# Kernel tuning notes

Hardware: AMD Instinct MI355X
Metric: run time of the kernel (lower is better)

Reference implementation:

```python
import jax, jax.numpy as jnp
import numpy as np

NUM_ENVS = 16384
N = 12          # decision vars (4 legs x 3D force)
M_CON = 24      # 4 SOC cones (3 each) + 12-dim hardtanh box
A_MIN, A_MAX = -10.0, 10.0
ALPHA, BETA = 1.0, 1.0


def setup_inputs() -> dict:
    key = jax.random.key(0)
    k1, k2, k3, k4 = jax.random.split(key, 4)
    Mw = jax.random.normal(k1, (NUM_ENVS, N, N), dtype=jnp.float32) / np.sqrt(N)
    # P must be SPD for inv/solve as in the original QP setup
    P = Mw @ jnp.swapaxes(Mw, -1, -2) + jnp.eye(N, dtype=jnp.float32)
    q = jax.random.normal(k2, (NUM_ENVS, N), dtype=jnp.float32)
    H = jax.random.normal(k3, (NUM_ENVS, M_CON, N), dtype=jnp.float32) * 0.5
    b = jax.random.normal(k4, (NUM_ENVS, M_CON), dtype=jnp.float32)
    contact_filter = jnp.ones((NUM_ENVS, M_CON), dtype=jnp.float32)
    return {"P": P, "q": q, "H": H, "b": b, "contact_filter": contact_filter, "iters": 100}


def _project(z, cf):
    # z: [B, m, 1]. Faithful to torch: project_onto_soc's only in-place effect on z
    # is z_part *= (z_part[:, 2:3] > 0); the full cone projection result is
    # discarded (returned but never written back). Then hardtanh box, then contact filter.
    Bsz = z.shape[0]
    soc = z[:, :12].reshape(Bsz, 4, 3)               # 4 cones of dim 3
    soc = soc * (soc[:, :, 2:3] > 0)                 # zero cone block if z-component <= 0
    box = jnp.clip(z[:, 12:24], A_MIN, A_MAX)        # hardtanh
    z = jnp.concatenate([soc.reshape(Bsz, 12, 1), box], axis=1)
    return z * cf


def reference(P, q, H, b, contact_filter, iters):
    m = H.shape[1]
    q_ = q[..., None]                                # [B, n, 1]
    b_ = b[..., None]                                # [B, m, 1]
    cf = contact_filter[..., None]                   # [B, m, 1]
    Ht = jnp.swapaxes(H, -1, -2)
    I = jnp.eye(m, dtype=P.dtype)
    Fm = I - H @ jnp.linalg.inv(P + Ht @ H) @ Ht     # [B, m, m]
    mu = Fm @ (H @ jnp.linalg.solve(P, q_) - b_)     # [B, m, 1]
    A = jnp.concatenate([
        jnp.concatenate([Fm, BETA * Fm], axis=2),
        jnp.concatenate([ALPHA * (I - 2.0 * Fm), I - 2.0 * ALPHA * BETA * Fm], axis=2),
    ], axis=1)                                       # [B, 2m, 2m]
    Bv = jnp.concatenate([BETA * mu, -2.0 * ALPHA * BETA * mu], axis=1)  # [B, 2m, 1]

    def step(lz, _):
        lz = A @ lz + Bv
        lz = jnp.concatenate([lz[:, :m], _project(lz[:, m:], cf)], axis=1)
        return lz, None

    lz0 = jnp.zeros((P.shape[0], 2 * m, 1), dtype=P.dtype)
    lz, _ = jax.lax.scan(step, lz0, None, length=iters)
    x = jnp.linalg.pinv(H) @ (lz[:, m:] - b_)        # [B, n, 1]
    return x, lz
```

## Files before the change

### kernel.cpp

```cpp
#include <hip/hip_runtime.h>

#define EPB 32
#define BLOCK 256
#define HS 292
#define GS 148
#define SS 28

#define WFENCE() __builtin_amdgcn_wave_barrier()

#define DPP_XOR1 0xB1
#define DPP_XOR2 0x4E
#define DPP_HMIR 0x141

constexpr int GMAP[8] = {0, 1, 2, 3, 7, 6, 5, 4};

typedef float f2 __attribute__((ext_vector_type(2)));

__device__ __forceinline__ f2 pkfma(f2 a, f2 b, f2 c) {
  return __builtin_elementwise_fma(a, b, c);
}

#define FMA4(acc, f, s)                                         \
  acc = fmaf((f).x, (s).x,                                      \
        fmaf((f).y, (s).y,                                      \
        fmaf((f).z, (s).z,                                      \
        fmaf((f).w, (s).w, (acc)))))

#define VFMA(acc, s, v)                                         \
  { (acc).x = fmaf((s), (v).x, (acc).x);                        \
    (acc).y = fmaf((s), (v).y, (acc).y);                        \
    (acc).z = fmaf((s), (v).z, (acc).z);                        \
    (acc).w = fmaf((s), (v).w, (acc).w); }

#define ADD4(A, B) { (A).x += (B).x; (A).y += (B).y; (A).z += (B).z; (A).w += (B).w; }

template<int CTRL>
__device__ __forceinline__ float dppv(float v) {
  return __int_as_float(__builtin_amdgcn_update_dpp(
      0, __float_as_int(v), CTRL, 0xF, 0xF, true));
}

template<int K>
__device__ __forceinline__ float getel(const float4& a, const float4& b, const float4& c) {
  if constexpr (K == 0) return a.x; else if constexpr (K == 1) return a.y;
  else if constexpr (K == 2) return a.z; else if constexpr (K == 3) return a.w;
  else if constexpr (K == 4) return b.x; else if constexpr (K == 5) return b.y;
  else if constexpr (K == 6) return b.z; else if constexpr (K == 7) return b.w;
  else if constexpr (K == 8) return c.x; else if constexpr (K == 9) return c.y;
  else if constexpr (K == 10) return c.z; else return c.w;
}
template<int K>
__device__ __forceinline__ void setel(float4& a, float4& b, float4& c, float v) {
  if constexpr (K == 0) a.x = v; else if constexpr (K == 1) a.y = v;
  else if constexpr (K == 2) a.z = v; else if constexpr (K == 3) a.w = v;
  else if constexpr (K == 4) b.x = v; else if constexpr (K == 5) b.y = v;
  else if constexpr (K == 6) b.z = v; else if constexpr (K == 7) b.w = v;
  else if constexpr (K == 8) c.x = v; else if constexpr (K == 9) c.y = v;
  else if constexpr (K == 10) c.z = v; else c.w = v;
}

template<int S>
__device__ __forceinline__ void putS2(f2* m, float v) {
  if constexpr ((S & 1) == 0) m[S / 2].x = v; else m[S / 2].y = v;
}

#define PMQ(pm, Q) make_float4(pm[2*(Q)].x, pm[2*(Q)].y, pm[2*(Q)+1].x, pm[2*(Q)+1].y)

__device__ __forceinline__ float dot12(float4 a0, float4 a1, float4 a2,
                                       const float* p) {
  const float4* p4 = (const float4*)p;
  float4 b0 = p4[0], b1 = p4[1], b2 = p4[2];
  float acc = 0.f;
  FMA4(acc, a0, b0); FMA4(acc, a1, b1); FMA4(acc, a2, b2);
  return acc;
}

template<int K>
__device__ __forceinline__ void pivot_pub(float4& a, float4& b, float4& c, float* piv) {
  float ip = 1.0f / getel<K>(a, b, c);
  setel<K>(a, b, c, 1.0f);
  a.x *= ip; a.y *= ip; a.z *= ip; a.w *= ip;
  b.x *= ip; b.y *= ip; b.z *= ip; b.w *= ip;
  c.x *= ip; c.y *= ip; c.z *= ip; c.w *= ip;
  float4* pv = (float4*)piv;
  pv[0] = a; pv[1] = b; pv[2] = c;
}

#define ELIM(f, A, B, C)                                              \
  { (A).x = fmaf(-(f), p0.x, (A).x); (A).y = fmaf(-(f), p0.y, (A).y); \
    (A).z = fmaf(-(f), p0.z, (A).z); (A).w = fmaf(-(f), p0.w, (A).w); \
    (B).x = fmaf(-(f), p1.x, (B).x); (B).y = fmaf(-(f), p1.y, (B).y); \
    (B).z = fmaf(-(f), p1.z, (B).z); (B).w = fmaf(-(f), p1.w, (B).w); \
    (C).x = fmaf(-(f), p2.x, (C).x); (C).y = fmaf(-(f), p2.y, (C).y); \
    (C).z = fmaf(-(f), p2.z, (C).z); (C).w = fmaf(-(f), p2.w, (C).w); }

template<int K>
__device__ __forceinline__ void rgj_step(float4& a0, float4& b0, float4& c0,
                                         float4& a1, float4& b1, float4& c1,
                                         float* piv, int t) {
  if constexpr (K < 8) {
    if (t == K) pivot_pub<K>(a0, b0, c0, piv);
  } else {
    if (t == K - 8) pivot_pub<K>(a1, b1, c1, piv);
  }
  WFENCE();
  const float4* pv = (const float4*)piv;
  float4 p0 = pv[0], p1 = pv[1], p2 = pv[2];
  {
    const bool own = (K < 8) && (t == K);
    float cur = getel<K>(a0, b0, c0);
    float f = own ? 0.0f : cur;
    setel<K>(a0, b0, c0, own ? cur : 0.0f);
    ELIM(f, a0, b0, c0);
  }
  {
    const bool own = (K >= 8) && (t == K - 8);
    float cur = getel<K>(a1, b1, c1);
    float f = own ? 0.0f : cur;
    setel<K>(a1, b1, c1, own ? cur : 0.0f);
    ELIM(f, a1, b1, c1);
  }
  WFENCE();
}

template<int K>
__device__ __forceinline__ void rgj_all(float4& a0, float4& b0, float4& c0,
                                        float4& a1, float4& b1, float4& c1,
                                        float* piv, int t) {
  rgj_step<K>(a0, b0, c0, a1, b1, c1, piv, t);
  if constexpr (K < 11) rgj_all<K + 1>(a0, b0, c0, a1, b1, c1, piv, t);
}

__device__ __forceinline__ void gram_rows(const float* myH, int t, int i1,
    float4& a0, float4& b0, float4& c0, float4& a1, float4& b1, float4& c1) {
  a0 = make_float4(0.f, 0.f, 0.f, 0.f);
  b0 = a0; c0 = a0; a1 = a0; b1 = a0; c1 = a0;
#pragma unroll
  for (int k = 0; k < 24; ++k) {
    const float4* hk = (const float4*)(myH + k * 12);
    float4 h0 = hk[0], h1 = hk[1], h2 = hk[2];
    float f0 = myH[k * 12 + t];
    float f1 = myH[k * 12 + i1];
    VFMA(a0, f0, h0); VFMA(b0, f0, h1); VFMA(c0, f0, h2);
    VFMA(a1, f1, h0); VFMA(b1, f1, h1); VFMA(c1, f1, h2);
  }
}

template<int g, int k>
__device__ __forceinline__ void slot3(const float* myH, int t,
    const float4* W0, const float4* W1, const float4* W2,
    f2* P0, f2* P1, f2* P2) {
  const int c = 3 * (t ^ GMAP[g]) + k;
  const float4* hc = (const float4*)(myH + c * 12);
  float4 h0 = hc[0], h1 = hc[1], h2 = hc[2];
  float d0 = 0.f, d1 = 0.f, d2 = 0.f;
  FMA4(d0, h0, W0[0]); FMA4(d0, h1, W0[1]); FMA4(d0, h2, W0[2]);
  FMA4(d1, h0, W1[0]); FMA4(d1, h1, W1[1]); FMA4(d1, h2, W1[2]);
  FMA4(d2, h0, W2[0]); FMA4(d2, h1, W2[1]); FMA4(d2, h2, W2[2]);
  constexpr int S = 3 * g + k;
  putS2<S>(P0, ((g == 0 && k == 0) ? 1.0f : 0.0f) - d0);
  putS2<S>(P1, ((g == 0 && k == 1) ? 1.0f : 0.0f) - d1);
  putS2<S>(P2, ((g == 0 && k == 2) ? 1.0f : 0.0f) - d2);
}

template<int S>
__device__ __forceinline__ float bgat(const float* bB, int t) {
  constexpr int g = S / 3, k = S % 3;
  return bB[3 * (t ^ GMAP[g]) + k];
}

__global__ __attribute__((amdgpu_flat_work_group_size(BLOCK, BLOCK),
                          amdgpu_waves_per_eu(1, 4)))
void pdhg_kernel(const float* __restrict__ P, const float* __restrict__ q,
                 const float* __restrict__ H, const float* __restrict__ b,
                 const float* __restrict__ cf, const int* __restrict__ itp,
                 float* __restrict__ out, int Btot) {
  __shared__ __align__(16) float sH[EPB * HS];
  __shared__ __align__(16) float sGi[EPB * GS];
  __shared__ __align__(16) float sB[EPB * SS];
  __shared__ __align__(16) float sAux[EPB * SS];

  const int tid  = threadIdx.x;
  const int wq   = tid >> 6;
  const int lane = tid & 63;
  const int e    = wq * 8 + (lane >> 3);
  const int t    = lane & 7;
  const int env  = blockIdx.x * EPB + e;
  const int envW0 = blockIdx.x * EPB + wq * 8;
  const int niter = itp[0];
  const int r0w = 3 * t;
  const int i1 = (t < 4) ? t + 8 : t;

  {
    const float4* gH = (const float4*)(H + (size_t)envW0 * 288);
#pragma unroll
    for (int rep = 0; rep < 9; ++rep) {
      int i = lane + rep * 64;
      int ee = i / 72, off = i - ee * 72;
      *(float4*)&sH[(wq * 8 + ee) * HS + off * 4] = gH[i];
    }
    const float4* gP = (const float4*)(P + (size_t)envW0 * 144);
#pragma unroll
    for (int rep = 0; rep < 4; ++rep) {
      int i = lane + rep * 64;
      int ee = i / 36, off = i - ee * 36;
      *(float4*)&sGi[(wq * 8 + ee) * GS + off * 4] = gP[i];
    }
    { int i = lane + 256; if (lane < 32) {
        int ee = i / 36, off = i - ee * 36;
        *(float4*)&sGi[(wq * 8 + ee) * GS + off * 4] = gP[i]; } }
    const float4* gq = (const float4*)(q + (size_t)envW0 * 12);
    if (lane < 24) {
      int ee = lane / 3, off = lane - ee * 3;
      *(float4*)&sAux[(wq * 8 + ee) * SS + off * 4] = gq[lane];
    }
    const float4* gb = (const float4*)(b + (size_t)envW0 * 24);
    if (lane < 48) {
      int ee = lane / 6, off = lane - ee * 6;
      *(float4*)&sB[(wq * 8 + ee) * SS + off * 4] = gb[lane];
    }
  }
  WFENCE();

  const float* myH = &sH[e * HS];
  float* giB  = &sGi[e * GS];
  float* auxB = &sAux[e * SS];
  float* bBm  = &sB[e * SS];
  const float* bB = bBm;

  float4 g0a, g0b, g0c, g1a, g1b, g1c;
  gram_rows(myH, t, i1, g0a, g0b, g0c, g1a, g1b, g1c);
  {
    const float4* p0 = (const float4*)(giB + t * 12);
    const float4* p1 = (const float4*)(giB + i1 * 12);
    float4 q0 = p0[0], q1 = p0[1], q2 = p0[2];
    float4 r0 = p1[0], r1 = p1[1], r2 = p1[2];
    ADD4(g0a, q0); ADD4(g0b, q1); ADD4(g0c, q2);
    ADD4(g1a, r0); ADD4(g1b, r1); ADD4(g1c, r2);
  }
  rgj_all<0>(g0a, g0b, g0c, g1a, g1b, g1c, auxB + 12, t);

  {
    float4* w0 = (float4*)(giB + t * 12);
    w0[0] = g0a; w0[1] = g0b; w0[2] = g0c;
    if (t < 4) {
      float4* w1 = (float4*)(giB + (t + 8) * 12);
      w1[0] = g1a; w1[1] = g1b; w1[2] = g1c;
    }
  }
  float y0 = dot12(g0a, g0b, g0c, auxB);
  float y1 = dot12(g1a, g1b, g1c, auxB);
  WFENCE();
  auxB[12 + t] = y0;
  if (t < 4) auxB[20 + t] = y1;
  WFENCE();

  float4 hr0[3], hr1[3], hr2[3];
  { const float4* p = (const float4*)(myH + (r0w + 0) * 12); hr0[0]=p[0]; hr0[1]=p[1]; hr0[2]=p[2]; }
  { const float4* p = (const float4*)(myH + (r0w + 1) * 12); hr1[0]=p[0]; hr1[1]=p[1]; hr1[2]=p[2]; }
  { const float4* p = (const float4*)(myH + (r0w + 2) * 12); hr2[0]=p[0]; hr2[1]=p[1]; hr2[2]=p[2]; }
  float u0, u1, u2;
  {
    const float4* y4 = (const float4*)(auxB + 12);
    float4 ya = y4[0], yb = y4[1], yc = y4[2];
    u0 = 0.f; FMA4(u0, hr0[0], ya); FMA4(u0, hr0[1], yb); FMA4(u0, hr0[2], yc);
    u1 = 0.f; FMA4(u1, hr1[0], ya); FMA4(u1, hr1[1], yb); FMA4(u1, hr1[2], yc);
    u2 = 0.f; FMA4(u2, hr2[0], ya); FMA4(u2, hr2[1], yb); FMA4(u2, hr2[2], yc);
  }

  float4 W0[3], W1[3], W2[3];
  W0[0] = make_float4(0.f,0.f,0.f,0.f); W0[1] = W0[0]; W0[2] = W0[0];
  W1[0] = W0[0]; W1[1] = W0[0]; W1[2] = W0[0];
  W2[0] = W0[0]; W2[1] = W0[0]; W2[2] = W0[0];
#define ACC_W(c, EX)                                                   \
  { const float4* g4 = (const float4*)(giB + (c) * 12);                \
    float4 r0 = g4[0], r1 = g4[1], r2 = g4[2];                         \
    float k0 = hr0[(c) >> 2].EX, k1 = hr1[(c) >> 2].EX, k2 = hr2[(c) >> 2].EX; \
    VFMA(W0[0], k0, r0); VFMA(W0[1], k0, r1); VFMA(W0[2], k0, r2);     \
    VFMA(W1[0], k1, r0); VFMA(W1[1], k1, r1); VFMA(W1[2], k1, r2);     \
    VFMA(W2[0], k2, r0); VFMA(W2[1], k2, r1); VFMA(W2[2], k2, r2); }
  ACC_W(0, x) ACC_W(1, y) ACC_W(2,  z) ACC_W(3,  w)
  ACC_W(4, x) ACC_W(5, y) ACC_W(6,  z) ACC_W(7,  w)
  ACC_W(8, x) ACC_W(9, y) ACC_W(10, z) ACC_W(11, w)
#undef ACC_W

  f2 pm0[12], pm1[12], pm2[12];
#define SL(g, k) slot3<g, k>(myH, t, W0, W1, W2, pm0, pm1, pm2);
  SL(0,0) SL(0,1) SL(0,2)  SL(1,0) SL(1,1) SL(1,2)
  SL(2,0) SL(2,1) SL(2,2)  SL(3,0) SL(3,1) SL(3,2)
  SL(4,0) SL(4,1) SL(4,2)  SL(5,0) SL(5,1) SL(5,2)
  SL(6,0) SL(6,1) SL(6,2)  SL(7,0) SL(7,1) SL(7,2)
#undef SL

  float mu0, mu1, mu2;
  {
    float4 bg0 = make_float4(bgat<0>(bB,t),  bgat<1>(bB,t),  bgat<2>(bB,t),  bgat<3>(bB,t));
    float4 bg1 = make_float4(bgat<4>(bB,t),  bgat<5>(bB,t),  bgat<6>(bB,t),  bgat<7>(bB,t));
    float4 bg2 = make_float4(bgat<8>(bB,t),  bgat<9>(bB,t),  bgat<10>(bB,t), bgat<11>(bB,t));
    float4 bg3 = make_float4(bgat<12>(bB,t), bgat<13>(bB,t), bgat<14>(bB,t), bgat<15>(bB,t));
    float4 bg4 = make_float4(bgat<16>(bB,t), bgat<17>(bB,t), bgat<18>(bB,t), bgat<19>(bB,t));
    float4 bg5 = make_float4(bgat<20>(bB,t), bgat<21>(bB,t), bgat<22>(bB,t), bgat<23>(bB,t));
    float d0 = 0.f, d1 = 0.f, d2 = 0.f;
    FMA4(d0, PMQ(pm0,0), bg0); FMA4(d1, PMQ(pm1,0), bg0); FMA4(d2, PMQ(pm2,0), bg0);
    FMA4(d0, PMQ(pm0,1), bg1); FMA4(d1, PMQ(pm1,1), bg1); FMA4(d2, PMQ(pm2,1), bg1);
    FMA4(d0, PMQ(pm0,2), bg2); FMA4(d1, PMQ(pm1,2), bg2); FMA4(d2, PMQ(pm2,2), bg2);
    FMA4(d0, PMQ(pm0,3), bg3); FMA4(d1, PMQ(pm1,3), bg3); FMA4(d2, PMQ(pm2,3), bg3);
    FMA4(d0, PMQ(pm0,4), bg4); FMA4(d1, PMQ(pm1,4), bg4); FMA4(d2, PMQ(pm2,4), bg4);
    FMA4(d0, PMQ(pm0,5), bg5); FMA4(d1, PMQ(pm1,5), bg5); FMA4(d2, PMQ(pm2,5), bg5);
    mu0 = u0 - d0;
    mu1 = u1 - d1;
    mu2 = u2 - d2;
  }
  float cfr0 = cf[(size_t)env * 24 + r0w];
  float cfr1 = cf[(size_t)env * 24 + r0w + 1];
  float cfr2 = cf[(size_t)env * 24 + r0w + 2];

  const float plo  = (t < 4) ? -3.0e38f : -10.0f;
  const float phi  = (t < 4) ?  3.0e38f :  10.0f;
  const float pthr = (t < 4) ? 0.0f     : -3.0e38f;
  float l0 = 0.f, l1 = 0.f, l2 = 0.f, z0 = 0.f, z1 = 0.f, z2 = 0.f;
#pragma unroll 2
  for (int it = 0; it < niter; ++it) {
    float s0 = l0 + z0, s1 = l1 + z1, s2 = l2 + z2;
    float g3  = dppv<DPP_XOR1>(s0), g4  = dppv<DPP_XOR1>(s1), g5  = dppv<DPP_XOR1>(s2);
    float g6  = dppv<DPP_XOR2>(s0), g7  = dppv<DPP_XOR2>(s1), g8  = dppv<DPP_XOR2>(s2);
    float g12 = dppv<DPP_HMIR>(s0), g13 = dppv<DPP_HMIR>(s1), g14 = dppv<DPP_HMIR>(s2);
    f2 vp0 = {s0, s1};
    f2 A0 = {mu0, 0.f}, A1 = {mu1, 0.f}, A2 = {mu2, 0.f};
    A0 = pkfma(pm0[0], vp0, A0); A1 = pkfma(pm1[0], vp0, A1); A2 = pkfma(pm2[0], vp0, A2);
    float g9  = dppv<DPP_XOR2>(g3),  g10 = dppv<DPP_XOR2>(g4),  g11 = dppv<DPP_XOR2>(g5);
    float g15 = dppv<DPP_HMIR>(g3),  g16 = dppv<DPP_HMIR>(g4),  g17 = dppv<DPP_HMIR>(g5);
    float g18 = dppv<DPP_HMIR>(g6),  g19 = dppv<DPP_HMIR>(g7),  g20 = dppv<DPP_HMIR>(g8);
    f2 vp1 = {s2, g3}, vp2 = {g4, g5}, vp3 = {g6, g7};
    A0 = pkfma(pm0[1], vp1, A0); A1 = pkfma(pm1[1], vp1, A1); A2 = pkfma(pm2[1], vp1, A2);
    A0 = pkfma(pm0[2], vp2, A0); A1 = pkfma(pm1[2], vp2, A1); A2 = pkfma(pm2[2], vp2, A2);
    A0 = pkfma(pm0[3], vp3, A0); A1 = pkfma(pm1[3], vp3, A1); A2 = pkfma(pm2[3], vp3, A2);
    float g21 = dppv<DPP_HMIR>(g9), g22 = dppv<DPP_HMIR>(g10), g23 = dppv<DPP_HMIR>(g11);
    f2 vp4 = {g8, g9}, vp5 = {g10, g11};
    A0 = pkfma(pm0[4], vp4, A0); A1 = pkfma(pm1[4], vp4, A1); A2 = pkfma(pm2[4], vp4, A2);
    A0 = pkfma(pm0[5], vp5, A0); A1 = pkfma(pm1[5], vp5, A1); A2 = pkfma(pm2[5], vp5, A2);
    f2 vp6 = {g12, g13}, vp7 = {g14, g15}, vp8 = {g16, g17}, vp9 = {g18, g19};
    f2 B0 = {0.f, 0.f}, B1 = {0.f, 0.f}, B2 = {0.f, 0.f};
    B0 = pkfma(pm0[6], vp6, B0); B1 = pkfma(pm1[6], vp6, B1); B2 = pkfma(pm2[6], vp6, B2);
    B0 = pkfma(pm0[7], vp7, B0); B1 = pkfma(pm1[7], vp7, B1); B2 = pkfma(pm2[7], vp7, B2);
    B0 = pkfma(pm0[8], vp8, B0); B1 = pkfma(pm1[8], vp8, B1); B2 = pkfma(pm2[8], vp8, B2);
    B0 = pkfma(pm0[9], vp9, B0); B1 = pkfma(pm1[9], vp9, B1); B2 = pkfma(pm2[9], vp9, B2);
    f2 vp10 = {g20, g21}, vp11 = {g22, g23};
    B0 = pkfma(pm0[10], vp10, B0); B1 = pkfma(pm1[10], vp10, B1); B2 = pkfma(pm2[10], vp10, B2);
    B0 = pkfma(pm0[11], vp11, B0); B1 = pkfma(pm1[11], vp11, B1); B2 = pkfma(pm2[11], vp11, B2);
    f2 C0 = A0 + B0, C1 = A1 + B1, C2 = A2 + B2;
    float w0 = C0.x + C0.y, w1 = C1.x + C1.y, w2 = C2.x + C2.y;
    float zp0 = fmaf(-2.0f, w0, s0);
    float zp1 = fmaf(-2.0f, w1, s1);
    float zp2 = fmaf(-2.0f, w2, s2);
    l0 = w0; l1 = w1; l2 = w2;
    bool gt = zp2 > pthr;
    float e0 = gt ? cfr0 : 0.0f;
    float e1 = gt ? cfr1 : 0.0f;
    float e2 = gt ? cfr2 : 0.0f;
    z0 = __builtin_amdgcn_fmed3f(zp0, plo, phi) * e0;
    z1 = __builtin_amdgcn_fmed3f(zp1, plo, phi) * e1;
    z2 = __builtin_amdgcn_fmed3f(zp2, plo, phi) * e2;
  }

  float* xout  = out;
  float* lzout = out + (size_t)Btot * 12;
  lzout[(size_t)env * 48 + r0w]          = l0;
  lzout[(size_t)env * 48 + r0w + 1]      = l1;
  lzout[(size_t)env * 48 + r0w + 2]      = l2;
  lzout[(size_t)env * 48 + 24 + r0w]     = z0;
  lzout[(size_t)env * 48 + 24 + r0w + 1] = z1;
  lzout[(size_t)env * 48 + 24 + r0w + 2] = z2;

  float bo0 = bB[r0w];
  float bo1 = bB[r0w + 1];
  float bo2 = bB[r0w + 2];
  WFENCE();
  auxB[r0w]     = z0 - bo0;
  auxB[r0w + 1] = z1 - bo1;
  auxB[r0w + 2] = z2 - bo2;
  WFENCE();

  float rv0 = 0.f, rv8 = 0.f;
  {
    const float4* a4 = (const float4*)auxB;
    float4 au0 = a4[0], au1 = a4[1], au2 = a4[2], au3 = a4[3], au4 = a4[4], au5 = a4[5];
#define RVS(k, AV) { rv0 = fmaf(myH[(k) * 12 + t],  (AV), rv0);   \
                     rv8 = fmaf(myH[(k) * 12 + i1], (AV), rv8); }
    RVS(0,  au0.x) RVS(1,  au0.y) RVS(2,  au0.z) RVS(3,  au0.w)
    RVS(4,  au1.x) RVS(5,  au1.y) RVS(6,  au1.z) RVS(7,  au1.w)
    RVS(8,  au2.x) RVS(9,  au2.y) RVS(10, au2.z) RVS(11, au2.w)
    RVS(12, au3.x) RVS(13, au3.y) RVS(14, au3.z) RVS(15, au3.w)
    RVS(16, au4.x) RVS(17, au4.y) RVS(18, au4.z) RVS(19, au4.w)
    RVS(20, au5.x) RVS(21, au5.y) RVS(22, au5.z) RVS(23, au5.w)
#undef RVS
  }

  gram_rows(myH, t, i1, g0a, g0b, g0c, g1a, g1b, g1c);
  WFENCE();
  auxB[t] = rv0;
  if (t < 4) auxB[t + 8] = rv8;
  WFENCE();
  rgj_all<0>(g0a, g0b, g0c, g1a, g1b, g1c, bBm, t);

  xout[(size_t)env * 12 + t] = dot12(g0a, g0b, g0c, auxB);
  if (t < 4)
    xout[(size_t)env * 12 + t + 8] = dot12(g1a, g1b, g1c, auxB);
}

extern "C" void kernel_launch(void* const* d_in, const int* in_sizes, int n_in,
                              void* d_out, int out_size, void* d_ws, size_t ws_size,
                              hipStream_t stream) {
  const float* P  = (const float*)d_in[0];
  const float* q  = (const float*)d_in[1];
  const float* H  = (const float*)d_in[2];
  const float* b  = (const float*)d_in[3];
  const float* cf = (const float*)d_in[4];
  const int*   it = (const int*)d_in[5];
  float* out = (float*)d_out;
  const int B = in_sizes[1] / 12;
  const int grid = B / EPB;
  pdhg_kernel<<<grid, BLOCK, 0, stream>>>(P, q, H, b, cf, it, out, B);
}
```

Measured before the change: 139.6 us.

## Process two environments per lane group to interleave independent iteration chains

Each 8-lane group now handles two environments (A and B) instead of one, with the block shrunk to 128 threads so EPB stays 32. The 100-step iteration interleaves the two environments' DPP shuffles and packed FMAs to hide latency through instruction-level parallelism. The DPP gather also changes: g9..g11 come from a single quad-permute DPP on s instead of a chained XOR2 of g3, which shortens the dependency chain. In exchange, per-thread register pressure roughly doubles (two sets of 36 packed coefficients), which may lower occupancy or cause spills, and there are half as many threads per block.

Result: slower. 182.2 us (+30.6%).

```diff
diff --git a/kernel.cpp b/kernel.cpp
--- a/kernel.cpp
+++ b/kernel.cpp
@@ -1,7 +1,7 @@
 #include <hip/hip_runtime.h>
 
 #define EPB 32
-#define BLOCK 256
+#define BLOCK 128
 #define HS 292
 #define GS 148
 #define SS 28
@@ -10,6 +10,7 @@
 
 #define DPP_XOR1 0xB1
 #define DPP_XOR2 0x4E
+#define DPP_QP3  0x1B
 #define DPP_HMIR 0x141
 
 constexpr int GMAP[8] = {0, 1, 2, 3, 7, 6, 5, 4};
@@ -169,6 +170,197 @@
   return bB[3 * (t ^ GMAP[g]) + k];
 }
 
+struct ES {
+  f2 pm0[12], pm1[12], pm2[12];
+  float mu0, mu1, mu2;
+  float cf0, cf1, cf2;
+  float l0, l1, l2, z0, z1, z2;
+};
+
+__device__ __forceinline__ void build_env(ES& S, const float* myH, float* gi,
+                                          float* aux, const float* bB,
+                                          const float* cfp, int t, int i1, int r0w) {
+  float4 g0a, g0b, g0c, g1a, g1b, g1c;
+  gram_rows(myH, t, i1, g0a, g0b, g0c, g1a, g1b, g1c);
+  {
+    const float4* p0 = (const float4*)(gi + t * 12);
+    const float4* p1 = (const float4*)(gi + i1 * 12);
+    float4 q0 = p0[0], q1 = p0[1], q2 = p0[2];
+    float4 r0 = p1[0], r1 = p1[1], r2 = p1[2];
+    ADD4(g0a, q0); ADD4(g0b, q1); ADD4(g0c, q2);
+    ADD4(g1a, r0); ADD4(g1b, r1); ADD4(g1c, r2);
+  }
+  rgj_all<0>(g0a, g0b, g0c, g1a, g1b, g1c, aux + 12, t);
+  {
+    float4* w0 = (float4*)(gi + t * 12);
+    w0[0] = g0a; w0[1] = g0b; w0[2] = g0c;
+    if (t < 4) {
+      float4* w1 = (float4*)(gi + (t + 8) * 12);
+      w1[0] = g1a; w1[1] = g1b; w1[2] = g1c;
+    }
+  }
+  float y0 = dot12(g0a, g0b, g0c, aux);
+  float y1 = dot12(g1a, g1b, g1c, aux);
+  WFENCE();
+  aux[12 + t] = y0;
+  if (t < 4) aux[20 + t] = y1;
+  WFENCE();
+
+  float4 hr0[3], hr1[3], hr2[3];
+  { const float4* p = (const float4*)(myH + (r0w + 0) * 12); hr0[0]=p[0]; hr0[1]=p[1]; hr0[2]=p[2]; }
+  { const float4* p = (const float4*)(myH + (r0w + 1) * 12); hr1[0]=p[0]; hr1[1]=p[1]; hr1[2]=p[2]; }
+  { const float4* p = (const float4*)(myH + (r0w + 2) * 12); hr2[0]=p[0]; hr2[1]=p[1]; hr2[2]=p[2]; }
+  float u0, u1, u2;
+  {
+    const float4* y4 = (const float4*)(aux + 12);
+    float4 ya = y4[0], yb = y4[1], yc = y4[2];
+    u0 = 0.f; FMA4(u0, hr0[0], ya); FMA4(u0, hr0[1], yb); FMA4(u0, hr0[2], yc);
+    u1 = 0.f; FMA4(u1, hr1[0], ya); FMA4(u1, hr1[1], yb); FMA4(u1, hr1[2], yc);
+    u2 = 0.f; FMA4(u2, hr2[0], ya); FMA4(u2, hr2[1], yb); FMA4(u2, hr2[2], yc);
+  }
+
+  float4 W0[3], W1[3], W2[3];
+  W0[0] = make_float4(0.f,0.f,0.f,0.f); W0[1] = W0[0]; W0[2] = W0[0];
+  W1[0] = W0[0]; W1[1] = W0[0]; W1[2] = W0[0];
+  W2[0] = W0[0]; W2[1] = W0[0]; W2[2] = W0[0];
+#define ACC_W(c, EX)                                                   \
+  { const float4* g4 = (const float4*)(gi + (c) * 12);                 \
+    float4 r0 = g4[0], r1 = g4[1], r2 = g4[2];                         \
+    float k0 = hr0[(c) >> 2].EX, k1 = hr1[(c) >> 2].EX, k2 = hr2[(c) >> 2].EX; \
+    VFMA(W0[0], k0, r0); VFMA(W0[1], k0, r1); VFMA(W0[2], k0, r2);     \
+    VFMA(W1[0], k1, r0); VFMA(W1[1], k1, r1); VFMA(W1[2], k1, r2);     \
+    VFMA(W2[0], k2, r0); VFMA(W2[1], k2, r1); VFMA(W2[2], k2, r2); }
+  ACC_W(0, x) ACC_W(1, y) ACC_W(2,  z) ACC_W(3,  w)
+  ACC_W(4, x) ACC_W(5, y) ACC_W(6,  z) ACC_W(7,  w)
+  ACC_W(8, x) ACC_W(9, y) ACC_W(10, z) ACC_W(11, w)
+#undef ACC_W
+
+#define SL(g, k) slot3<g, k>(myH, t, W0, W1, W2, S.pm0, S.pm1, S.pm2);
+  SL(0,0) SL(0,1) SL(0,2)  SL(1,0) SL(1,1) SL(1,2)
+  SL(2,0) SL(2,1) SL(2,2)  SL(3,0) SL(3,1) SL(3,2)
+  SL(4,0) SL(4,1) SL(4,2)  SL(5,0) SL(5,1) SL(5,2)
+  SL(6,0) SL(6,1) SL(6,2)  SL(7,0) SL(7,1) SL(7,2)
+#undef SL
+
+  {
+    float4 bg0 = make_float4(bgat<0>(bB,t),  bgat<1>(bB,t),  bgat<2>(bB,t),  bgat<3>(bB,t));
+    float4 bg1 = make_float4(bgat<4>(bB,t),  bgat<5>(bB,t),  bgat<6>(bB,t),  bgat<7>(bB,t));
+    float4 bg2 = make_float4(bgat<8>(bB,t),  bgat<9>(bB,t),  bgat<10>(bB,t), bgat<11>(bB,t));
+    float4 bg3 = make_float4(bgat<12>(bB,t), bgat<13>(bB,t), bgat<14>(bB,t), bgat<15>(bB,t));
+    float4 bg4 = make_float4(bgat<16>(bB,t), bgat<17>(bB,t), bgat<18>(bB,t), bgat<19>(bB,t));
+    float4 bg5 = make_float4(bgat<20>(bB,t), bgat<21>(bB,t), bgat<22>(bB,t), bgat<23>(bB,t));
+    float d0 = 0.f, d1 = 0.f, d2 = 0.f;
+    FMA4(d0, PMQ(S.pm0,0), bg0); FMA4(d1, PMQ(S.pm1,0), bg0); FMA4(d2, PMQ(S.pm2,0), bg0);
+    FMA4(d0, PMQ(S.pm0,1), bg1); FMA4(d1, PMQ(S.pm1,1), bg1); FMA4(d2, PMQ(S.pm2,1), bg1);
+    FMA4(d0, PMQ(S.pm0,2), bg2); FMA4(d1, PMQ(S.pm1,2), bg2); FMA4(d2, PMQ(S.pm2,2), bg2);
+    FMA4(d0, PMQ(S.pm0,3), bg3); FMA4(d1, PMQ(S.pm1,3), bg3); FMA4(d2, PMQ(S.pm2,3), bg3);
+    FMA4(d0, PMQ(S.pm0,4), bg4); FMA4(d1, PMQ(S.pm1,4), bg4); FMA4(d2, PMQ(S.pm2,4), bg4);
+    FMA4(d0, PMQ(S.pm0,5), bg5); FMA4(d1, PMQ(S.pm1,5), bg5); FMA4(d2, PMQ(S.pm2,5), bg5);
+    S.mu0 = u0 - d0;
+    S.mu1 = u1 - d1;
+    S.mu2 = u2 - d2;
+  }
+  S.cf0 = cfp[0]; S.cf1 = cfp[1]; S.cf2 = cfp[2];
+  S.l0 = S.l1 = S.l2 = S.z0 = S.z1 = S.z2 = 0.f;
+}
+
+__device__ __forceinline__ void epi_env(ES& S, const float* myH, float* gi,
+                                        float* aux, float* bBm,
+                                        float* xout, float* lzout,
+                                        int env_, int t, int i1, int r0w) {
+  lzout[(size_t)env_ * 48 + r0w]          = S.l0;
+  lzout[(size_t)env_ * 48 + r0w + 1]      = S.l1;
+  lzout[(size_t)env_ * 48 + r0w + 2]      = S.l2;
+  lzout[(size_t)env_ * 48 + 24 + r0w]     = S.z0;
+  lzout[(size_t)env_ * 48 + 24 + r0w + 1] = S.z1;
+  lzout[(size_t)env_ * 48 + 24 + r0w + 2] = S.z2;
+
+  float bo0 = bBm[r0w];
+  float bo1 = bBm[r0w + 1];
+  float bo2 = bBm[r0w + 2];
+  WFENCE();
+  aux[r0w]     = S.z0 - bo0;
+  aux[r0w + 1] = S.z1 - bo1;
+  aux[r0w + 2] = S.z2 - bo2;
+  WFENCE();
+
+  float rv0 = 0.f, rv8 = 0.f;
+  {
+    const float4* a4 = (const float4*)aux;
+    float4 au0 = a4[0], au1 = a4[1], au2 = a4[2], au3 = a4[3], au4 = a4[4], au5 = a4[5];
+#define RVS(k, AV) { rv0 = fmaf(myH[(k) * 12 + t],  (AV), rv0);   \
+                     rv8 = fmaf(myH[(k) * 12 + i1], (AV), rv8); }
+    RVS(0,  au0.x) RVS(1,  au0.y) RVS(2,  au0.z) RVS(3,  au0.w)
+    RVS(4,  au1.x) RVS(5,  au1.y) RVS(6,  au1.z) RVS(7,  au1.w)
+    RVS(8,  au2.x) RVS(9,  au2.y) RVS(10, au2.z) RVS(11, au2.w)
+    RVS(12, au3.x) RVS(13, au3.y) RVS(14, au3.z) RVS(15, au3.w)
+    RVS(16, au4.x) RVS(17, au4.y) RVS(18, au4.z) RVS(19, au4.w)
+    RVS(20, au5.x) RVS(21, au5.y) RVS(22, au5.z) RVS(23, au5.w)
+#undef RVS
+  }
+
+  float4 g0a, g0b, g0c, g1a, g1b, g1c;
+  gram_rows(myH, t, i1, g0a, g0b, g0c, g1a, g1b, g1c);
+  WFENCE();
+  aux[t] = rv0;
+  if (t < 4) aux[t + 8] = rv8;
+  WFENCE();
+  rgj_all<0>(g0a, g0b, g0c, g1a, g1b, g1c, bBm, t);
+
+  xout[(size_t)env_ * 12 + t] = dot12(g0a, g0b, g0c, aux);
+  if (t < 4)
+    xout[(size_t)env_ * 12 + t + 8] = dot12(g1a, g1b, g1c, aux);
+}
+
+#define IT_S(E) \
+  float E##s0 = E.l0 + E.z0, E##s1 = E.l1 + E.z1, E##s2 = E.l2 + E.z2;
+
+#define IT_L1(E) \
+  float E##g3  = dppv<DPP_XOR1>(E##s0), E##g4  = dppv<DPP_XOR1>(E##s1), E##g5  = dppv<DPP_XOR1>(E##s2); \
+  float E##g6  = dppv<DPP_XOR2>(E##s0), E##g7  = dppv<DPP_XOR2>(E##s1), E##g8  = dppv<DPP_XOR2>(E##s2); \
+  float E##g9  = dppv<DPP_QP3>(E##s0),  E##g10 = dppv<DPP_QP3>(E##s1),  E##g11 = dppv<DPP_QP3>(E##s2);  \
+  float E##g12 = dppv<DPP_HMIR>(E##s0), E##g13 = dppv<DPP_HMIR>(E##s1), E##g14 = dppv<DPP_HMIR>(E##s2);
+
+#define IT_L2(E) \
+  float E##g15 = dppv<DPP_HMIR>(E##g3), E##g16 = dppv<DPP_HMIR>(E##g4), E##g17 = dppv<DPP_HMIR>(E##g5); \
+  float E##g18 = dppv<DPP_HMIR>(E##g6), E##g19 = dppv<DPP_HMIR>(E##g7), E##g20 = dppv<DPP_HMIR>(E##g8); \
+  float E##g21 = dppv<DPP_HMIR>(E##g9), E##g22 = dppv<DPP_HMIR>(E##g10), E##g23 = dppv<DPP_HMIR>(E##g11);
+
+#define IT_FMA(E) \
+  f2 E##vp0 = {E##s0, E##s1},   E##vp1 = {E##s2, E##g3},   E##vp2 = {E##g4, E##g5};   \
+  f2 E##vp3 = {E##g6, E##g7},   E##vp4 = {E##g8, E##g9},   E##vp5 = {E##g10, E##g11}; \
+  f2 E##vp6 = {E##g12, E##g13}, E##vp7 = {E##g14, E##g15}, E##vp8 = {E##g16, E##g17}; \
+  f2 E##vp9 = {E##g18, E##g19}, E##vp10 = {E##g20, E##g21}, E##vp11 = {E##g22, E##g23}; \
+  f2 E##A0 = {E.mu0, 0.f}, E##A1 = {E.mu1, 0.f}, E##A2 = {E.mu2, 0.f}; \
+  f2 E##B0 = {0.f, 0.f}, E##B1 = {0.f, 0.f}, E##B2 = {0.f, 0.f}; \
+  E##A0 = pkfma(E.pm0[0], E##vp0, E##A0); E##A1 = pkfma(E.pm1[0], E##vp0, E##A1); E##A2 = pkfma(E.pm2[0], E##vp0, E##A2); \
+  E##A0 = pkfma(E.pm0[1], E##vp1, E##A0); E##A1 = pkfma(E.pm1[1], E##vp1, E##A1); E##A2 = pkfma(E.pm2[1], E##vp1, E##A2); \
+  E##A0 = pkfma(E.pm0[2], E##vp2, E##A0); E##A1 = pkfma(E.pm1[2], E##vp2, E##A1); E##A2 = pkfma(E.pm2[2], E##vp2, E##A2); \
+  E##A0 = pkfma(E.pm0[3], E##vp3, E##A0); E##A1 = pkfma(E.pm1[3], E##vp3, E##A1); E##A2 = pkfma(E.pm2[3], E##vp3, E##A2); \
+  E##A0 = pkfma(E.pm0[4], E##vp4, E##A0); E##A1 = pkfma(E.pm1[4], E##vp4, E##A1); E##A2 = pkfma(E.pm2[4], E##vp4, E##A2); \
+  E##A0 = pkfma(E.pm0[5], E##vp5, E##A0); E##A1 = pkfma(E.pm1[5], E##vp5, E##A1); E##A2 = pkfma(E.pm2[5], E##vp5, E##A2); \
+  E##B0 = pkfma(E.pm0[6], E##vp6, E##B0); E##B1 = pkfma(E.pm1[6], E##vp6, E##B1); E##B2 = pkfma(E.pm2[6], E##vp6, E##B2); \
+  E##B0 = pkfma(E.pm0[7], E##vp7, E##B0); E##B1 = pkfma(E.pm1[7], E##vp7, E##B1); E##B2 = pkfma(E.pm2[7], E##vp7, E##B2); \
+  E##B0 = pkfma(E.pm0[8], E##vp8, E##B0); E##B1 = pkfma(E.pm1[8], E##vp8, E##B1); E##B2 = pkfma(E.pm2[8], E##vp8, E##B2); \
+  E##B0 = pkfma(E.pm0[9], E##vp9, E##B0); E##B1 = pkfma(E.pm1[9], E##vp9, E##B1); E##B2 = pkfma(E.pm2[9], E##vp9, E##B2); \
+  E##B0 = pkfma(E.pm0[10], E##vp10, E##B0); E##B1 = pkfma(E.pm1[10], E##vp10, E##B1); E##B2 = pkfma(E.pm2[10], E##vp10, E##B2); \
+  E##B0 = pkfma(E.pm0[11], E##vp11, E##B0); E##B1 = pkfma(E.pm1[11], E##vp11, E##B1); E##B2 = pkfma(E.pm2[11], E##vp11, E##B2);
+
+#define IT_TAIL(E) \
+  f2 E##C0 = E##A0 + E##B0, E##C1 = E##A1 + E##B1, E##C2 = E##A2 + E##B2; \
+  float E##w0 = E##C0.x + E##C0.y, E##w1 = E##C1.x + E##C1.y, E##w2 = E##C2.x + E##C2.y; \
+  float E##zp0 = fmaf(-2.0f, E##w0, E##s0); \
+  float E##zp1 = fmaf(-2.0f, E##w1, E##s1); \
+  float E##zp2 = fmaf(-2.0f, E##w2, E##s2); \
+  E.l0 = E##w0; E.l1 = E##w1; E.l2 = E##w2; \
+  bool E##gt = E##zp2 > pthr; \
+  float E##e0 = E##gt ? E.cf0 : 0.0f; \
+  float E##e1 = E##gt ? E.cf1 : 0.0f; \
+  float E##e2 = E##gt ? E.cf2 : 0.0f; \
+  E.z0 = __builtin_amdgcn_fmed3f(E##zp0, plo, phi) * E##e0; \
+  E.z1 = __builtin_amdgcn_fmed3f(E##zp1, plo, phi) * E##e1; \
+  E.z2 = __builtin_amdgcn_fmed3f(E##zp2, plo, phi) * E##e2;
+
 __global__ __attribute__((amdgpu_flat_work_group_size(BLOCK, BLOCK),
                           amdgpu_waves_per_eu(1, 4)))
 void pdhg_kernel(const float* __restrict__ P, const float* __restrict__ q,
@@ -183,10 +375,13 @@
   const int tid  = threadIdx.x;
   const int wq   = tid >> 6;
   const int lane = tid & 63;
-  const int e    = wq * 8 + (lane >> 3);
+  const int g8   = lane >> 3;
   const int t    = lane & 7;
-  const int env  = blockIdx.x * EPB + e;
-  const int envW0 = blockIdx.x * EPB + wq * 8;
+  const int eA   = wq * 16 + g8;
+  const int eB   = eA + 8;
+  const int envA = blockIdx.x * EPB + eA;
+  const int envB = envA + 8;
+  const int envW0 = blockIdx.x * EPB + wq * 16;
   const int niter = itp[0];
   const int r0w = 3 * t;
   const int i1 = (t < 4) ? t + 8 : t;
@@ -194,218 +389,66 @@
   {
     const float4* gH = (const float4*)(H + (size_t)envW0 * 288);
 #pragma unroll
-    for (int rep = 0; rep < 9; ++rep) {
+    for (int rep = 0; rep < 18; ++rep) {
       int i = lane + rep * 64;
       int ee = i / 72, off = i - ee * 72;
-      *(float4*)&sH[(wq * 8 + ee) * HS + off * 4] = gH[i];
+      *(float4*)&sH[(wq * 16 + ee) * HS + off * 4] = gH[i];
     }
     const float4* gP = (const float4*)(P + (size_t)envW0 * 144);
 #pragma unroll
-    for (int rep = 0; rep < 4; ++rep) {
+    for (int rep = 0; rep < 9; ++rep) {
       int i = lane + rep * 64;
       int ee = i / 36, off = i - ee * 36;
-      *(float4*)&sGi[(wq * 8 + ee) * GS + off * 4] = gP[i];
+      *(float4*)&sGi[(wq * 16 + ee) * GS + off * 4] = gP[i];
     }
-    { int i = lane + 256; if (lane < 32) {
-        int ee = i / 36, off = i - ee * 36;
-        *(float4*)&sGi[(wq * 8 + ee) * GS + off * 4] = gP[i]; } }
     const float4* gq = (const float4*)(q + (size_t)envW0 * 12);
-    if (lane < 24) {
+    if (lane < 48) {
       int ee = lane / 3, off = lane - ee * 3;
-      *(float4*)&sAux[(wq * 8 + ee) * SS + off * 4] = gq[lane];
+      *(float4*)&sAux[(wq * 16 + ee) * SS + off * 4] = gq[lane];
     }
     const float4* gb = (const float4*)(b + (size_t)envW0 * 24);
-    if (lane < 48) {
-      int ee = lane / 6, off = lane - ee * 6;
-      *(float4*)&sB[(wq * 8 + ee) * SS + off * 4] = gb[lane];
+    {
+      int i = lane;
+      int ee = i / 6, off = i - ee * 6;
+      *(float4*)&sB[(wq * 16 + ee) * SS + off * 4] = gb[i];
+      if (lane < 32) {
+        i = lane + 64;
+        ee = i / 6; off = i - ee * 6;
+        *(float4*)&sB[(wq * 16 + ee) * SS + off * 4] = gb[i];
+      }
     }
   }
   WFENCE();
 
-  const float* myH = &sH[e * HS];
-  float* giB  = &sGi[e * GS];
-  float* auxB = &sAux[e * SS];
-  float* bBm  = &sB[e * SS];
-  const float* bB = bBm;
-
-  float4 g0a, g0b, g0c, g1a, g1b, g1c;
-  gram_rows(myH, t, i1, g0a, g0b, g0c, g1a, g1b, g1c);
-  {
-    const float4* p0 = (const float4*)(giB + t * 12);
-    const float4* p1 = (const float4*)(giB + i1 * 12);
-    float4 q0 = p0[0], q1 = p0[1], q2 = p0[2];
-    float4 r0 = p1[0], r1 = p1[1], r2 = p1[2];
-    ADD4(g0a, q0); ADD4(g0b, q1); ADD4(g0c, q2);
-    ADD4(g1a, r0); ADD4(g1b, r1); ADD4(g1c, r2);
-  }
-  rgj_all<0>(g0a, g0b, g0c, g1a, g1b, g1c, auxB + 12, t);
-
-  {
-    float4* w0 = (float4*)(giB + t * 12);
-    w0[0] = g0a; w0[1] = g0b; w0[2] = g0c;
-    if (t < 4) {
-      float4* w1 = (float4*)(giB + (t + 8) * 12);
-      w1[0] = g1a; w1[1] = g1b; w1[2] = g1c;
-    }
-  }
-  float y0 = dot12(g0a, g0b, g0c, auxB);
-  float y1 = dot12(g1a, g1b, g1c, auxB);
-  WFENCE();
-  auxB[12 + t] = y0;
-  if (t < 4) auxB[20 + t] = y1;
-  WFENCE();
-
-  float4 hr0[3], hr1[3], hr2[3];
-  { const float4* p = (const float4*)(myH + (r0w + 0) * 12); hr0[0]=p[0]; hr0[1]=p[1]; hr0[2]=p[2]; }
-  { const float4* p = (const float4*)(myH + (r0w + 1) * 12); hr1[0]=p[0]; hr1[1]=p[1]; hr1[2]=p[2]; }
-  { const float4* p = (const float4*)(myH + (r0w + 2) * 12); hr2[0]=p[0]; hr2[1]=p[1]; hr2[2]=p[2]; }
-  float u0, u1, u2;
-  {
-    const float4* y4 = (const float4*)(auxB + 12);
-    float4 ya = y4[0], yb = y4[1], yc = y4[2];
-    u0 = 0.f; FMA4(u0, hr0[0], ya); FMA4(u0, hr0[1], yb); FMA4(u0, hr0[2], yc);
-    u1 = 0.f; FMA4(u1, hr1[0], ya); FMA4(u1, hr1[1], yb); FMA4(u1, hr1[2], yc);
-    u2 = 0.f; FMA4(u2, hr2[0], ya); FMA4(u2, hr2[1], yb); FMA4(u2, hr2[2], yc);
-  }
-
-  float4 W0[3], W1[3], W2[3];
-  W0[0] = make_float4(0.f,0.f,0.f,0.f); W0[1] = W0[0]; W0[2] = W0[0];
-  W1[0] = W0[0]; W1[1] = W0[0]; W1[2] = W0[0];
-  W2[0] = W0[0]; W2[1] = W0[0]; W2[2] = W0[0];
-#define ACC_W(c, EX)                                                   \
-  { const float4* g4 = (const float4*)(giB + (c) * 12);                \
-    float4 r0 = g4[0], r1 = g4[1], r2 = g4[2];                         \
-    float k0 = hr0[(c) >> 2].EX, k1 = hr1[(c) >> 2].EX, k2 = hr2[(c) >> 2].EX; \
-    VFMA(W0[0], k0, r0); VFMA(W0[1], k0, r1); VFMA(W0[2], k0, r2);     \
-    VFMA(W1[0], k1, r0); VFMA(W1[1], k1, r1); VFMA(W1[2], k1, r2);     \
-    VFMA(W2[0], k2, r0); VFMA(W2[1], k2, r1); VFMA(W2[2], k2, r2); }
-  ACC_W(0, x) ACC_W(1, y) ACC_W(2,  z) ACC_W(3,  w)
-  ACC_W(4, x) ACC_W(5, y) ACC_W(6,  z) ACC_W(7,  w)
-  ACC_W(8, x) ACC_W(9, y) ACC_W(10, z) ACC_W(11, w)
-#undef ACC_W
-
-  f2 pm0[12], pm1[12], pm2[12];
-#define SL(g, k) slot3<g, k>(myH, t, W0, W1, W2, pm0, pm1, pm2);
-  SL(0,0) SL(0,1) SL(0,2)  SL(1,0) SL(1,1) SL(1,2)
-  SL(2,0) SL(2,1) SL(2,2)  SL(3,0) SL(3,1) SL(3,2)
-  SL(4,0) SL(4,1) SL(4,2)  SL(5,0) SL(5,1) SL(5,2)
-  SL(6,0) SL(6,1) SL(6,2)  SL(7,0) SL(7,1) SL(7,2)
-#undef SL
-
-  float mu0, mu1, mu2;
-  {
-    float4 bg0 = make_float4(bgat<0>(bB,t),  bgat<1>(bB,t),  bgat<2>(bB,t),  bgat<3>(bB,t));
-    float4 bg1 = make_float4(bgat<4>(bB,t),  bgat<5>(bB,t),  bgat<6>(bB,t),  bgat<7>(bB,t));
-    float4 bg2 = make_float4(bgat<8>(bB,t),  bgat<9>(bB,t),  bgat<10>(bB,t), bgat<11>(bB,t));
-    float4 bg3 = make_float4(bgat<12>(bB,t), bgat<13>(bB,t), bgat<14>(bB,t), bgat<15>(bB,t));
-    float4 bg4 = make_float4(bgat<16>(bB,t), bgat<17>(bB,t), bgat<18>(bB,t), bgat<19>(bB,t));
-    float4 bg5 = make_float4(bgat<20>(bB,t), bgat<21>(bB,t), bgat<22>(bB,t), bgat<23>(bB,t));
-    float d0 = 0.f, d1 = 0.f, d2 = 0.f;
-    FMA4(d0, PMQ(pm0,0), bg0); FMA4(d1, PMQ(pm1,0), bg0); FMA4(d2, PMQ(pm2,0), bg0);
-    FMA4(d0, PMQ(pm0,1), bg1); FMA4(d1, PMQ(pm1,1), bg1); FMA4(d2, PMQ(pm2,1), bg1);
-    FMA4(d0, PMQ(pm0,2), bg2); FMA4(d1, PMQ(pm1,2), bg2); FMA4(d2, PMQ(pm2,2), bg2);
-    FMA4(d0, PMQ(pm0,3), bg3); FMA4(d1, PMQ(pm1,3), bg3); FMA4(d2, PMQ(pm2,3), bg3);
-    FMA4(d0, PMQ(pm0,4), bg4); FMA4(d1, PMQ(pm1,4), bg4); FMA4(d2, PMQ(pm2,4), bg4);
-    FMA4(d0, PMQ(pm0,5), bg5); FMA4(d1, PMQ(pm1,5), bg5); FMA4(d2, PMQ(pm2,5), bg5);
-    mu0 = u0 - d0;
-    mu1 = u1 - d1;
-    mu2 = u2 - d2;
-  }
-  float cfr0 = cf[(size_t)env * 24 + r0w];
-  float cfr1 = cf[(size_t)env * 24 + r0w + 1];
-  float cfr2 = cf[(size_t)env * 24 + r0w + 2];
+  const float* myHA = &sH[eA * HS];
+  const float* myHB = &sH[eB * HS];
+  float* giA  = &sGi[eA * GS];
+  float* giBp = &sGi[eB * GS];
+  float* auxA = &sAux[eA * SS];
+  float* auxBp = &sAux[eB * SS];
+  float* bA   = &sB[eA * SS];
+  float* bBp  = &sB[eB * SS];
+
+  ES A, B;
+  build_env(A, myHA, giA, auxA, bA, cf + (size_t)envA * 24 + r0w, t, i1, r0w);
+  build_env(B, myHB, giBp, auxBp, bBp, cf + (size_t)envB * 24 + r0w, t, i1, r0w);
 
   const float plo  = (t < 4) ? -3.0e38f : -10.0f;
   const float phi  = (t < 4) ?  3.0e38f :  10.0f;
   const float pthr = (t < 4) ? 0.0f     : -3.0e38f;
-  float l0 = 0.f, l1 = 0.f, l2 = 0.f, z0 = 0.f, z1 = 0.f, z2 = 0.f;
-#pragma unroll 2
+#pragma unroll 1
   for (int it = 0; it < niter; ++it) {
-    float s0 = l0 + z0, s1 = l1 + z1, s2 = l2 + z2;
-    float g3  = dppv<DPP_XOR1>(s0), g4  = dppv<DPP_XOR1>(s1), g5  = dppv<DPP_XOR1>(s2);
-    float g6  = dppv<DPP_XOR2>(s0), g7  = dppv<DPP_XOR2>(s1), g8  = dppv<DPP_XOR2>(s2);
-    float g12 = dppv<DPP_HMIR>(s0), g13 = dppv<DPP_HMIR>(s1), g14 = dppv<DPP_HMIR>(s2);
-    f2 vp0 = {s0, s1};
-    f2 A0 = {mu0, 0.f}, A1 = {mu1, 0.f}, A2 = {mu2, 0.f};
-    A0 = pkfma(pm0[0], vp0, A0); A1 = pkfma(pm1[0], vp0, A1); A2 = pkfma(pm2[0], vp0, A2);
-    float g9  = dppv<DPP_XOR2>(g3),  g10 = dppv<DPP_XOR2>(g4),  g11 = dppv<DPP_XOR2>(g5);
-    float g15 = dppv<DPP_HMIR>(g3),  g16 = dppv<DPP_HMIR>(g4),  g17 = dppv<DPP_HMIR>(g5);
-    float g18 = dppv<DPP_HMIR>(g6),  g19 = dppv<DPP_HMIR>(g7),  g20 = dppv<DPP_HMIR>(g8);
-    f2 vp1 = {s2, g3}, vp2 = {g4, g5}, vp3 = {g6, g7};
-    A0 = pkfma(pm0[1], vp1, A0); A1 = pkfma(pm1[1], vp1, A1); A2 = pkfma(pm2[1], vp1, A2);
-    A0 = pkfma(pm0[2], vp2, A0); A1 = pkfma(pm1[2], vp2, A1); A2 = pkfma(pm2[2], vp2, A2);
-    A0 = pkfma(pm0[3], vp3, A0); A1 = pkfma(pm1[3], vp3, A1); A2 = pkfma(pm2[3], vp3, A2);
-    float g21 = dppv<DPP_HMIR>(g9), g22 = dppv<DPP_HMIR>(g10), g23 = dppv<DPP_HMIR>(g11);
-    f2 vp4 = {g8, g9}, vp5 = {g10, g11};
-    A0 = pkfma(pm0[4], vp4, A0); A1 = pkfma(pm1[4], vp4, A1); A2 = pkfma(pm2[4], vp4, A2);
-    A0 = pkfma(pm0[5], vp5, A0); A1 = pkfma(pm1[5], vp5, A1); A2 = pkfma(pm2[5], vp5, A2);
-    f2 vp6 = {g12, g13}, vp7 = {g14, g15}, vp8 = {g16, g17}, vp9 = {g18, g19};
-    f2 B0 = {0.f, 0.f}, B1 = {0.f, 0.f}, B2 = {0.f, 0.f};
-    B0 = pkfma(pm0[6], vp6, B0); B1 = pkfma(pm1[6], vp6, B1); B2 = pkfma(pm2[6], vp6, B2);
-    B0 = pkfma(pm0[7], vp7, B0); B1 = pkfma(pm1[7], vp7, B1); B2 = pkfma(pm2[7], vp7, B2);
-    B0 = pkfma(pm0[8], vp8, B0); B1 = pkfma(pm1[8], vp8, B1); B2 = pkfma(pm2[8], vp8, B2);
-    B0 = pkfma(pm0[9], vp9, B0); B1 = pkfma(pm1[9], vp9, B1); B2 = pkfma(pm2[9], vp9, B2);
-    f2 vp10 = {g20, g21}, vp11 = {g22, g23};
-    B0 = pkfma(pm0[10], vp10, B0); B1 = pkfma(pm1[10], vp10, B1); B2 = pkfma(pm2[10], vp10, B2);
-    B0 = pkfma(pm0[11], vp11, B0); B1 = pkfma(pm1[11], vp11, B1); B2 = pkfma(pm2[11], vp11, B2);
-    f2 C0 = A0 + B0, C1 = A1 + B1, C2 = A2 + B2;
-    float w0 = C0.x + C0.y, w1 = C1.x + C1.y, w2 = C2.x + C2.y;
-    float zp0 = fmaf(-2.0f, w0, s0);
-    float zp1 = fmaf(-2.0f, w1, s1);
-    float zp2 = fmaf(-2.0f, w2, s2);
-    l0 = w0; l1 = w1; l2 = w2;
-    bool gt = zp2 > pthr;
-    float e0 = gt ? cfr0 : 0.0f;
-    float e1 = gt ? cfr1 : 0.0f;
-    float e2 = gt ? cfr2 : 0.0f;
-    z0 = __builtin_amdgcn_fmed3f(zp0, plo, phi) * e0;
-    z1 = __builtin_amdgcn_fmed3f(zp1, plo, phi) * e1;
-    z2 = __builtin_amdgcn_fmed3f(zp2, plo, phi) * e2;
+    IT_S(A)  IT_S(B)
+    IT_L1(A) IT_L1(B)
+    IT_L2(A) IT_L2(B)
+    IT_FMA(A) IT_FMA(B)
+    IT_TAIL(A) IT_TAIL(B)
   }
 
   float* xout  = out;
   float* lzout = out + (size_t)Btot * 12;
-  lzout[(size_t)env * 48 + r0w]          = l0;
-  lzout[(size_t)env * 48 + r0w + 1]      = l1;
-  lzout[(size_t)env * 48 + r0w + 2]      = l2;
-  lzout[(size_t)env * 48 + 24 + r0w]     = z0;
-  lzout[(size_t)env * 48 + 24 + r0w + 1] = z1;
-  lzout[(size_t)env * 48 + 24 + r0w + 2] = z2;
-
-  float bo0 = bB[r0w];
-  float bo1 = bB[r0w + 1];
-  float bo2 = bB[r0w + 2];
-  WFENCE();
-  auxB[r0w]     = z0 - bo0;
-  auxB[r0w + 1] = z1 - bo1;
-  auxB[r0w + 2] = z2 - bo2;
-  WFENCE();
-
-  float rv0 = 0.f, rv8 = 0.f;
-  {
-    const float4* a4 = (const float4*)auxB;
-    float4 au0 = a4[0], au1 = a4[1], au2 = a4[2], au3 = a4[3], au4 = a4[4], au5 = a4[5];
-#define RVS(k, AV) { rv0 = fmaf(myH[(k) * 12 + t],  (AV), rv0);   \
-                     rv8 = fmaf(myH[(k) * 12 + i1], (AV), rv8); }
-    RVS(0,  au0.x) RVS(1,  au0.y) RVS(2,  au0.z) RVS(3,  au0.w)
-    RVS(4,  au1.x) RVS(5,  au1.y) RVS(6,  au1.z) RVS(7,  au1.w)
-    RVS(8,  au2.x) RVS(9,  au2.y) RVS(10, au2.z) RVS(11, au2.w)
-    RVS(12, au3.x) RVS(13, au3.y) RVS(14, au3.z) RVS(15, au3.w)
-    RVS(16, au4.x) RVS(17, au4.y) RVS(18, au4.z) RVS(19, au4.w)
-    RVS(20, au5.x) RVS(21, au5.y) RVS(22, au5.z) RVS(23, au5.w)
-#undef RVS
-  }
-
-  gram_rows(myH, t, i1, g0a, g0b, g0c, g1a, g1b, g1c);
-  WFENCE();
-  auxB[t] = rv0;
-  if (t < 4) auxB[t + 8] = rv8;
-  WFENCE();
-  rgj_all<0>(g0a, g0b, g0c, g1a, g1b, g1c, bBm, t);
-
-  xout[(size_t)env * 12 + t] = dot12(g0a, g0b, g0c, auxB);
-  if (t < 4)
-    xout[(size_t)env * 12 + t + 8] = dot12(g1a, g1b, g1c, auxB);
+  epi_env(A, myHA, giA, auxA, bA, xout, lzout, envA, t, i1, r0w);
+  epi_env(B, myHB, giBp, auxBp, bBp, xout, lzout, envB, t, i1, r0w);
 }
 
 extern "C" void kernel_launch(void* const* d_in, const int* in_sizes, int n_in,
```
